# Optimization experiments

Measured on AMD Instinct MI355X. Metric: run time of the kernel, lower is better.

## Reference

```python
import jax, jax.numpy as jnp
import numpy as np

NUM_HEADS = 32
HEAD_DIM = 128
NUM_KV_HEADS = 8
Q_LEN = 1024
MAX_SEQ = 4096
CACHE_BATCH = 4
SEQ_POS = 1024
BATCH_POS = 1


def setup_inputs() -> dict:
    key = jax.random.key(0)
    ks = jax.random.split(key, 6)
    query_state = jax.random.normal(ks[0], (1, NUM_HEADS, Q_LEN, HEAD_DIM), jnp.float32)
    key_state = jax.random.normal(ks[1], (1, NUM_KV_HEADS, Q_LEN, HEAD_DIM), jnp.float32)
    value_state = jax.random.normal(ks[2], (1, NUM_KV_HEADS, Q_LEN, HEAD_DIM), jnp.float32)
    past_key_state = jax.random.normal(ks[3], (CACHE_BATCH, NUM_KV_HEADS, MAX_SEQ, HEAD_DIM), jnp.float32)
    past_value_state = jax.random.normal(ks[4], (CACHE_BATCH, NUM_KV_HEADS, MAX_SEQ, HEAD_DIM), jnp.float32)
    # Causal prefill mask: query token i (global pos SEQ_POS+i) may attend to cache pos m <= SEQ_POS+i
    i = jnp.arange(Q_LEN)[:, None] + SEQ_POS
    j = jnp.arange(MAX_SEQ)[None, :]
    attn_mask = (j <= i).astype(jnp.float32)[None, None]  # [1,1,Q_LEN,MAX_SEQ]
    scale = jnp.array([1.0 / np.sqrt(HEAD_DIM)], jnp.float32)
    return {
        "query_state": query_state,
        "key_state": key_state,
        "value_state": value_state,
        "attn_mask": attn_mask,
        "batch_position": BATCH_POS,
        "past_key_state": past_key_state,
        "past_value_state": past_value_state,
        "seq_position": SEQ_POS,
        "scale": scale,
    }


def reference(query_state, key_state, value_state, attn_mask, batch_position,
              past_key_state, past_value_state, seq_position, scale):
    g = NUM_HEADS // NUM_KV_HEADS
    q_len = query_state.shape[2]
    # --- cache update (prefill: insert new K/V at [batch_position, :, seq_position:seq_position+q_len]) ---
    k_cache = jax.lax.dynamic_update_slice(past_key_state, key_state, (batch_position, 0, seq_position, 0))
    v_cache = jax.lax.dynamic_update_slice(past_value_state, value_state, (batch_position, 0, seq_position, 0))
    # --- grouped-query attention over the updated cache row ---
    q = query_state.reshape(1, NUM_KV_HEADS, g, q_len, HEAD_DIM)
    k = jax.lax.dynamic_slice_in_dim(k_cache, batch_position, 1, axis=0)[0]  # [kvh, MAX_SEQ, hd]
    v = jax.lax.dynamic_slice_in_dim(v_cache, batch_position, 1, axis=0)[0]
    scores = jnp.einsum('bkgqd,kmd->bkgqm', q, k) * scale[0]  # [1,kvh,g,q,MAX_SEQ]
    neg = jnp.finfo(scores.dtype).min
    scores = jnp.where(attn_mask[:, :, None] > 0.5, scores, neg)
    probs = jax.nn.softmax(scores, axis=-1)
    out = jnp.einsum('bkgqm,kmd->bkgqd', probs, v)  # [1,kvh,g,q,hd]
    out = out.reshape(1, NUM_HEADS, q_len, HEAD_DIM)
    attn_output = out.transpose(0, 2, 1, 3).reshape(1, q_len, NUM_HEADS * HEAD_DIM)
    return attn_output, k_cache, v_cache
```

## Files before the change

kernel.cpp:

```cpp
#include <hip/hip_runtime.h>

#define NH 32
#define KVHN 8
#define HD 128
#define QL 1024
#define MS 4096
#define KVB 64

typedef __bf16 bf16x8 __attribute__((ext_vector_type(8)));
typedef __bf16 bf16x4 __attribute__((ext_vector_type(4)));
typedef float f32x4 __attribute__((ext_vector_type(4)));
typedef float f32x16 __attribute__((ext_vector_type(16)));


__device__ __forceinline__ void gload16(const void* g, void* l) {
    __builtin_amdgcn_global_load_lds(
        (const __attribute__((address_space(1))) unsigned int*)g,
        (__attribute__((address_space(3))) unsigned int*)l, 16, 0, 0);
}

__device__ __forceinline__ unsigned int pk2(float a, float b) {
    union { __bf16 h; unsigned short u; } x, y;
    x.h = (__bf16)a; y.h = (__bf16)b;
    return (unsigned int)x.u | ((unsigned int)y.u << 16);
}

__device__ __forceinline__ float exp2fast(float x) {
    return __builtin_amdgcn_exp2f(x);
}

__global__ __launch_bounds__(256) void pack_kernel(
    const float4* __restrict__ kn, const float4* __restrict__ vn,
    const float4* __restrict__ pk, const float4* __restrict__ pv,
    const int* __restrict__ bp_p, const int* __restrict__ sp_p,
    __bf16* __restrict__ kbf, __bf16* __restrict__ vt)
{
    __shared__ float vtile[8][132];
    int li = blockIdx.x * 256 + threadIdx.x;
    int bp = *bp_p, sp = *sp_p;
    int d4  = li & 31;
    int pos = (li >> 5) & 4095;
    int kvh = li >> 17;
    float4 kv4, vv4;
    if (pos >= sp && pos < sp + QL) {
        int ns = (kvh * QL + (pos - sp)) * 32 + d4;
        kv4 = kn[ns]; vv4 = vn[ns];
    } else {
        int gi = (bp << 20) + li;
        kv4 = pk[gi]; vv4 = pv[gi];
    }
    {
        bf16x4 o;
        o[0] = (__bf16)kv4.x; o[1] = (__bf16)kv4.y;
        o[2] = (__bf16)kv4.z; o[3] = (__bf16)kv4.w;
        int c16 = d4 >> 1, half = d4 & 1;
        *(bf16x4*)(kbf + ((size_t)kvh * MS + pos) * HD
                       + ((c16 ^ (pos & 7)) * 8 + half * 4)) = o;
        *(float4*)&vtile[threadIdx.x >> 5][d4 * 4] = vv4;
    }
    __syncthreads();
    if (threadIdx.x < 128) {
        int d  = threadIdx.x;
        int p0 = (blockIdx.x * 8) & 4095;
        int pt = p0 >> 6, chk = (p0 & 63) >> 3;
        bf16x8 o;
        #pragma unroll
        for (int j = 0; j < 8; ++j) o[j] = (__bf16)vtile[j][d];
        *(bf16x8*)(vt + (((size_t)kvh * 64 + pt) * HD + d) * 64
                      + ((chk ^ (d & 7)) * 8)) = o;
    }
}

__global__ __launch_bounds__(256, 2) void mega_kernel(
    const float* __restrict__ q,
    const int* __restrict__ bp_p, const int* __restrict__ sp_p,
    const float* __restrict__ scale_p,
    const __bf16* __restrict__ kbf, const __bf16* __restrict__ vt,
    const float4* __restrict__ knf, const float4* __restrict__ vnf,
    const float4* __restrict__ pkf, const float4* __restrict__ pvf,
    float4* __restrict__ okf, float4* __restrict__ ovf,
    float* __restrict__ out)
{
    __shared__ __align__(16) unsigned char smem[65536];

    const int bid = blockIdx.x;
    const int tid = threadIdx.x;
    const int sp  = *sp_p;
    const int bp  = *bp_p;

    if (bid >= 512) {
        int cslot = bid - 512;
        const float4* csrc_new  = (cslot < 256) ? knf : vnf;
        const float4* csrc_past = (cslot < 256) ? pkf : pvf;
        float4*       cdst      = (cslot < 256) ? okf : ovf;
        const int     cbase     = (cslot & 255) * 16384;
        for (int s = 0; s < 16; ++s) {
            float4 t[4];
            #pragma unroll
            for (int jj = 0; jj < 4; ++jj) {
                int idx = cbase + s * 1024 + jj * 256 + tid;
                int d4  = idx & 31;
                int pos = (idx >> 5) & 4095;
                int ck  = (idx >> 17) & 7;
                int b   = idx >> 20;
                t[jj] = (b == bp && pos >= sp && pos < sp + QL)
                    ? csrc_new[(ck * QL + (pos - sp)) * 32 + d4]
                    : csrc_past[idx];
            }
            #pragma unroll
            for (int jj = 0; jj < 4; ++jj)
                cdst[cbase + s * 1024 + jj * 256 + tid] = t[jj];
        }
        return;
    }

    const float scl = *scale_p * 1.44269504088896340736f;

    int kvh = bid & 7;
    int inner = (bid & 255) >> 3;
    int headLocal = inner & 3;
    int j = inner >> 2;
    int qtile = (bid < 256) ? j : 15 - j;
    int head = kvh * 4 + headLocal;

    const int q0     = qtile * 64;
    const int wave   = tid >> 6;
    const int qsub   = wave & 1;
    const int kvhalf = wave >> 1;
    const int lane   = tid & 63;
    const int hi     = lane >> 5;
    const int c31    = lane & 31;
    const int qb     = q0 + qsub * 32;
    const int myq    = qb + c31;

    const unsigned char* krow = (const unsigned char*)(kbf + (size_t)kvh * MS * HD);
    const unsigned char* vrow = (const unsigned char*)(vt + (size_t)kvh * 64 * HD * 64);

    bf16x8 qf[8];
    #pragma unroll
    for (int dc = 0; dc < 8; ++dc) {
        const float* src = q + ((size_t)(head * QL + qb + c31) * HD + dc * 16 + hi * 8);
        float4 f0 = *(const float4*)src;
        float4 f1 = *(const float4*)(src + 4);
        bf16x8 v;
        v[0]=(__bf16)(f0.x*scl); v[1]=(__bf16)(f0.y*scl);
        v[2]=(__bf16)(f0.z*scl); v[3]=(__bf16)(f0.w*scl);
        v[4]=(__bf16)(f1.x*scl); v[5]=(__bf16)(f1.y*scl);
        v[6]=(__bf16)(f1.z*scl); v[7]=(__bf16)(f1.w*scl);
        qf[dc] = v;
    }

    f32x16 acc[4];
    #pragma unroll
    for (int dsub = 0; dsub < 4; ++dsub)
        #pragma unroll
        for (int r = 0; r < 16; ++r) acc[dsub][r] = 0.f;
    float m_run = -1e30f, l_run = 0.f;

    const int n_super = (sp + q0 + 64) >> 6;

    auto stage = [&](int buf, int t) {
        const unsigned char* kt = krow + (size_t)t * 16384;
        const unsigned char* vtile = vrow + (size_t)t * 16384;
        unsigned char* kl = smem + buf * 32768;
        unsigned char* vl = kl + 16384;
        #pragma unroll
        for (int p = 0; p < 4; ++p) {
            int off = p * 4096 + tid * 16;
            gload16(kt + off, kl + off);
            gload16(vtile + off, vl + off);
        }
    };

    int cur = 0;
    stage(0, 0);
    __syncthreads();

    for (int it = 0; it < n_super; ++it) {
        const int n0 = it * KVB + kvhalf * 32;
        if (it + 1 < n_super) stage(cur ^ 1, it + 1);

        const unsigned char* Ksm = smem + cur * 32768;
        const unsigned char* Vsm = Ksm + 16384;

        f32x16 st0, st1;
        #pragma unroll
        for (int r = 0; r < 16; ++r) { st0[r] = 0.f; st1[r] = 0.f; }
        int kr = kvhalf * 32 + c31;
        __builtin_amdgcn_s_setprio(1);
        #pragma unroll
        for (int dc = 0; dc < 4; ++dc) {
            bf16x8 ka = *(const bf16x8*)(Ksm + kr * 256 + (((2 * dc + hi) ^ (kr & 7)) << 4));
            st0 = __builtin_amdgcn_mfma_f32_32x32x16_bf16(ka, qf[dc], st0, 0, 0, 0);
            bf16x8 kb = *(const bf16x8*)(Ksm + kr * 256 + (((2 * (dc + 4) + hi) ^ (kr & 7)) << 4));
            st1 = __builtin_amdgcn_mfma_f32_32x32x16_bf16(kb, qf[dc + 4], st1, 0, 0, 0);
        }
        __builtin_amdgcn_s_setprio(0);
        f32x16 st = st0 + st1;

        const bool need_mask = (n0 + 31) > (sp + qb);
        if (need_mask) {
            #pragma unroll
            for (int r = 0; r < 16; ++r) {
                int kvg = n0 + (r & 3) + 8 * (r >> 2) + 4 * hi;
                if (kvg > sp + myq) st[r] = -1e30f;
            }
        }
        float m01 = fmaxf(fmaxf(st[0], st[1]), fmaxf(st[2], st[3]));
        float m23 = fmaxf(fmaxf(st[4], st[5]), fmaxf(st[6], st[7]));
        float m45 = fmaxf(fmaxf(st[8], st[9]), fmaxf(st[10], st[11]));
        float m67 = fmaxf(fmaxf(st[12], st[13]), fmaxf(st[14], st[15]));
        float mx = fmaxf(fmaxf(m01, m23), fmaxf(m45, m67));
        mx = fmaxf(mx, __shfl_xor(mx, 32));

        if (!__all(mx <= m_run + 8.0f)) {
            float nm = fmaxf(m_run, mx);
            float corr = exp2fast(m_run - nm);
            m_run = nm;
            l_run *= corr;
            #pragma unroll
            for (int r = 0; r < 16; ++r) {
                int qsrc = (r & 3) + 8 * (r >> 2) + 4 * hi;
                float cq = __shfl(corr, qsrc);
                acc[0][r] *= cq; acc[1][r] *= cq; acc[2][r] *= cq; acc[3][r] *= cq;
            }
        }

        #pragma unroll
        for (int r = 0; r < 16; ++r) st[r] = exp2fast(st[r] - m_run);
        {
            float s0 = (st[0] + st[1]) + (st[2] + st[3]);
            float s1 = (st[4] + st[5]) + (st[6] + st[7]);
            float s2 = (st[8] + st[9]) + (st[10] + st[11]);
            float s3 = (st[12] + st[13]) + (st[14] + st[15]);
            l_run += (s0 + s1) + (s2 + s3);
        }

        unsigned int loW[4], hiW[4];
        #pragma unroll
        for (int qd = 0; qd < 2; ++qd) {
            int b = qd * 8;
            loW[qd*2+0] = pk2(st[b+0], st[b+1]);
            loW[qd*2+1] = pk2(st[b+2], st[b+3]);
            hiW[qd*2+0] = pk2(st[b+4], st[b+5]);
            hiW[qd*2+1] = pk2(st[b+6], st[b+7]);
        }
        bf16x8 pfrag[2];
        #pragma unroll
        for (int qd = 0; qd < 2; ++qd) {
            unsigned int a0 = loW[qd*2+0], b0 = hiW[qd*2+0];
            unsigned int a1 = loW[qd*2+1], b1 = hiW[qd*2+1];
            asm("v_permlane32_swap_b32 %0, %1" : "+v"(a0), "+v"(b0));
            asm("v_permlane32_swap_b32 %0, %1" : "+v"(a1), "+v"(b1));
            union { unsigned int u[4]; bf16x8 v; } fu;
            fu.u[0] = a0; fu.u[1] = a1; fu.u[2] = b0; fu.u[3] = b1;
            pfrag[qd] = fu.v;
        }

        __builtin_amdgcn_s_setprio(1);
        #pragma unroll
        for (int dsub = 0; dsub < 4; ++dsub) {
            int vr = dsub * 32 + c31;
            #pragma unroll
            for (int qd = 0; qd < 2; ++qd) {
                int ksg = kvhalf * 2 + qd;
                bf16x8 vf = *(const bf16x8*)(Vsm + vr * 128 + (((ksg * 2 + hi) ^ (vr & 7)) << 4));
                acc[dsub] = __builtin_amdgcn_mfma_f32_32x32x16_bf16(pfrag[qd], vf, acc[dsub], 0, 0, 0);
            }
        }
        __builtin_amdgcn_s_setprio(0);

        __syncthreads();
        cur ^= 1;
    }

    float l_full = l_run + __shfl_xor(l_run, 32);
    float* mlm = (float*)smem;
    float* mll = (float*)smem + 128;
    if (hi == 0) { mlm[wave * 32 + c31] = m_run; mll[wave * 32 + c31] = l_full; }
    __syncthreads();
    int pw = wave ^ 2;
    float m_o = mlm[pw * 32 + c31];
    float l_o = mll[pw * 32 + c31];
    float m_n = fmaxf(m_run, m_o);
    float sc   = exp2fast(m_run - m_n);
    float sc_o = exp2fast(m_o - m_n);
    float linv = 1.0f / (l_full * sc + l_o * sc_o);
    float* Oex = (float*)(smem + 1024) + (size_t)qsub * 32 * 128;
    if (kvhalf) {
        #pragma unroll
        for (int r = 0; r < 16; ++r) {
            int qsrc = (r & 3) + 8 * (r >> 2) + 4 * hi;
            float s = __shfl(sc, qsrc);
            #pragma unroll
            for (int dsub = 0; dsub < 4; ++dsub)
                Oex[qsrc * 128 + dsub * 32 + c31] = acc[dsub][r] * s;
        }
    }
    __syncthreads();
    if (!kvhalf) {
        #pragma unroll
        for (int r = 0; r < 16; ++r) {
            int qsrc = (r & 3) + 8 * (r >> 2) + 4 * hi;
            float s  = __shfl(sc, qsrc);
            float lq = __shfl(linv, qsrc);
            float* orow = out + (size_t)(qb + qsrc) * (NH * HD) + head * HD;
            #pragma unroll
            for (int dsub = 0; dsub < 4; ++dsub)
                orow[dsub * 32 + c31] =
                    (acc[dsub][r] * s + Oex[qsrc * 128 + dsub * 32 + c31]) * lq;
        }
    }
}

extern "C" void kernel_launch(void* const* d_in, const int* in_sizes, int n_in,
                              void* d_out, int out_size, void* d_ws, size_t ws_size,
                              hipStream_t stream)
{
    const float* q_st   = (const float*)d_in[0];
    const float* k_new  = (const float*)d_in[1];
    const float* v_new  = (const float*)d_in[2];
    const int*   bp_p   = (const int*)d_in[4];
    const float* past_k = (const float*)d_in[5];
    const float* past_v = (const float*)d_in[6];
    const int*   sp_p   = (const int*)d_in[7];
    const float* scl_p  = (const float*)d_in[8];

    float* out_attn = (float*)d_out;
    float* out_k    = out_attn + (size_t)QL * NH * HD;
    float* out_v    = out_k + (size_t)4 * KVHN * MS * HD;

    __bf16* kbf = (__bf16*)d_ws;
    __bf16* vtw = kbf + (size_t)KVHN * MS * HD;

    pack_kernel<<<4096, 256, 0, stream>>>(
        (const float4*)k_new, (const float4*)v_new,
        (const float4*)past_k, (const float4*)past_v,
        bp_p, sp_p, kbf, vtw);

    mega_kernel<<<1024, 256, 0, stream>>>(
        q_st, bp_p, sp_p, scl_p, kbf, vtw,
        (const float4*)k_new, (const float4*)v_new,
        (const float4*)past_k, (const float4*)past_v,
        (float4*)out_k, (float4*)out_v, out_attn);
}
```

Before: 105.6 us.

## Co-schedule cache copy waves inside attention blocks with nontemporal loads/stores

Replaces the separate 512 copy-only blocks with 512-thread blocks in which the upper 256 threads copy the KV cache slices while the lower 256 threads compute attention. The copy waves step through the attention loop's barriers so that copy traffic is spread over the attention mainloop, and they use nontemporal loads and stores to avoid polluting cache. The barrier counts have to match the attention path exactly, and the larger blocks change occupancy and register limits via launch_bounds(512,4).

```diff
diff --git a/kernel.cpp b/kernel.cpp
--- a/kernel.cpp
+++ b/kernel.cpp
@@ -11,6 +11,7 @@
 typedef __bf16 bf16x4 __attribute__((ext_vector_type(4)));
 typedef float f32x4 __attribute__((ext_vector_type(4)));
 typedef float f32x16 __attribute__((ext_vector_type(16)));
+typedef unsigned int u32x4 __attribute__((ext_vector_type(4)));
 
 
 __device__ __forceinline__ void gload16(const void* g, void* l) {
@@ -27,6 +28,13 @@
 
 __device__ __forceinline__ float exp2fast(float x) {
     return __builtin_amdgcn_exp2f(x);
+}
+
+__device__ __forceinline__ u32x4 nt_load(const u32x4* p) {
+    return __builtin_nontemporal_load(p);
+}
+__device__ __forceinline__ void nt_store(u32x4* p, u32x4 v) {
+    __builtin_nontemporal_store(v, p);
 }
 
 __global__ __launch_bounds__(256) void pack_kernel(
@@ -71,7 +79,7 @@
     }
 }
 
-__global__ __launch_bounds__(256, 2) void mega_kernel(
+__global__ __launch_bounds__(512, 4) void mega_kernel(
     const float* __restrict__ q,
     const int* __restrict__ bp_p, const int* __restrict__ sp_p,
     const float* __restrict__ scale_p,
@@ -88,42 +96,67 @@
     const int sp  = *sp_p;
     const int bp  = *bp_p;
 
-    if (bid >= 512) {
-        int cslot = bid - 512;
-        const float4* csrc_new  = (cslot < 256) ? knf : vnf;
-        const float4* csrc_past = (cslot < 256) ? pkf : pvf;
-        float4*       cdst      = (cslot < 256) ? okf : ovf;
-        const int     cbase     = (cslot & 255) * 16384;
-        for (int s = 0; s < 16; ++s) {
-            float4 t[4];
-            #pragma unroll
-            for (int jj = 0; jj < 4; ++jj) {
-                int idx = cbase + s * 1024 + jj * 256 + tid;
-                int d4  = idx & 31;
-                int pos = (idx >> 5) & 4095;
-                int ck  = (idx >> 17) & 7;
-                int b   = idx >> 20;
-                t[jj] = (b == bp && pos >= sp && pos < sp + QL)
-                    ? csrc_new[(ck * QL + (pos - sp)) * 32 + d4]
-                    : csrc_past[idx];
-            }
-            #pragma unroll
-            for (int jj = 0; jj < 4; ++jj)
-                cdst[cbase + s * 1024 + jj * 256 + tid] = t[jj];
-        }
-        return;
-    }
-
-    const float scl = *scale_p * 1.44269504088896340736f;
-
     int kvh = bid & 7;
     int inner = (bid & 255) >> 3;
     int headLocal = inner & 3;
     int j = inner >> 2;
     int qtile = (bid < 256) ? j : 15 - j;
     int head = kvh * 4 + headLocal;
-
-    const int q0     = qtile * 64;
+    const int q0 = qtile * 64;
+    const int n_super = (sp + q0 + 64) >> 6;
+
+    if (tid >= 256) {
+        const int ctid = tid - 256;
+        const u32x4* csrc_new  = (const u32x4*)((bid < 256) ? knf : vnf);
+        const u32x4* csrc_past = (const u32x4*)((bid < 256) ? pkf : pvf);
+        u32x4*       cdst      = (u32x4*)((bid < 256) ? okf : ovf);
+        const int    cbase     = (bid & 255) * 16384;
+
+        __syncthreads();
+        for (int it = 0; it < n_super; ++it) {
+            if (it < 16) {
+                u32x4 t[4];
+                #pragma unroll
+                for (int jj = 0; jj < 4; ++jj) {
+                    int idx = cbase + it * 1024 + jj * 256 + ctid;
+                    int d4  = idx & 31;
+                    int pos = (idx >> 5) & 4095;
+                    int ck  = (idx >> 17) & 7;
+                    int b   = idx >> 20;
+                    t[jj] = (b == bp && pos >= sp && pos < sp + QL)
+                        ? nt_load(&csrc_new[(ck * QL + (pos - sp)) * 32 + d4])
+                        : nt_load(&csrc_past[idx]);
+                }
+                #pragma unroll
+                for (int jj = 0; jj < 4; ++jj)
+                    nt_store(&cdst[cbase + it * 1024 + jj * 256 + ctid], t[jj]);
+            }
+            __syncthreads();
+        }
+        for (int s = n_super; s < 16; ++s) {
+            u32x4 t[4];
+            #pragma unroll
+            for (int jj = 0; jj < 4; ++jj) {
+                int idx = cbase + s * 1024 + jj * 256 + ctid;
+                int d4  = idx & 31;
+                int pos = (idx >> 5) & 4095;
+                int ck  = (idx >> 17) & 7;
+                int b   = idx >> 20;
+                t[jj] = (b == bp && pos >= sp && pos < sp + QL)
+                    ? nt_load(&csrc_new[(ck * QL + (pos - sp)) * 32 + d4])
+                    : nt_load(&csrc_past[idx]);
+            }
+            #pragma unroll
+            for (int jj = 0; jj < 4; ++jj)
+                nt_store(&cdst[cbase + s * 1024 + jj * 256 + ctid], t[jj]);
+        }
+        __syncthreads();
+        __syncthreads();
+        return;
+    }
+
+    const float scl = *scale_p * 1.44269504088896340736f;
+
     const int wave   = tid >> 6;
     const int qsub   = wave & 1;
     const int kvhalf = wave >> 1;
@@ -156,8 +189,6 @@
         #pragma unroll
         for (int r = 0; r < 16; ++r) acc[dsub][r] = 0.f;
     float m_run = -1e30f, l_run = 0.f;
-
-    const int n_super = (sp + q0 + 64) >> 6;
 
     auto stage = [&](int buf, int t) {
         const unsigned char* kt = krow + (size_t)t * 16384;
@@ -338,7 +369,7 @@
         (const float4*)past_k, (const float4*)past_v,
         bp_p, sp_p, kbf, vtw);
 
-    mega_kernel<<<1024, 256, 0, stream>>>(
+    mega_kernel<<<512, 512, 0, stream>>>(
         q_st, bp_p, sp_p, scl_p, kbf, vtw,
         (const float4*)k_new, (const float4*)v_new,
         (const float4*)past_k, (const float4*)past_v,
```

Result: slower. 165.4 us (+56.6%).

## Load V fragments directly from global, halve LDS, interleave copy blocks

Applied to the files above, without the earlier changes.

V tiles are no longer staged through LDS. Each wave reads its V MFMA fragments straight from global memory into registers at the start of every iteration, and only K keeps the LDS double buffer. Shared memory drops to 32 KB, which may let more blocks fit per CU. The cache-copy blocks are now interleaved with the attention blocks in the grid and use nontemporal loads and stores. The partial-output exchange between waves is stored as bf16, which cuts LDS space but lowers the precision of that half of the accumulator.

```diff
diff --git a/kernel.cpp b/kernel.cpp
--- a/kernel.cpp
+++ b/kernel.cpp
@@ -11,6 +11,7 @@
 typedef __bf16 bf16x4 __attribute__((ext_vector_type(4)));
 typedef float f32x4 __attribute__((ext_vector_type(4)));
 typedef float f32x16 __attribute__((ext_vector_type(16)));
+typedef unsigned int u32x4 __attribute__((ext_vector_type(4)));
 
 
 __device__ __forceinline__ void gload16(const void* g, void* l) {
@@ -27,6 +28,13 @@
 
 __device__ __forceinline__ float exp2fast(float x) {
     return __builtin_amdgcn_exp2f(x);
+}
+
+__device__ __forceinline__ u32x4 nt_load(const u32x4* p) {
+    return __builtin_nontemporal_load(p);
+}
+__device__ __forceinline__ void nt_store(u32x4* p, u32x4 v) {
+    __builtin_nontemporal_store(v, p);
 }
 
 __global__ __launch_bounds__(256) void pack_kernel(
@@ -81,21 +89,21 @@
     float4* __restrict__ okf, float4* __restrict__ ovf,
     float* __restrict__ out)
 {
-    __shared__ __align__(16) unsigned char smem[65536];
+    __shared__ __align__(16) unsigned char smem[32768];
 
     const int bid = blockIdx.x;
     const int tid = threadIdx.x;
     const int sp  = *sp_p;
     const int bp  = *bp_p;
 
-    if (bid >= 512) {
-        int cslot = bid - 512;
-        const float4* csrc_new  = (cslot < 256) ? knf : vnf;
-        const float4* csrc_past = (cslot < 256) ? pkf : pvf;
-        float4*       cdst      = (cslot < 256) ? okf : ovf;
-        const int     cbase     = (cslot & 255) * 16384;
+    if ((bid >> 8) & 1) {
+        int cslot = (bid < 512) ? (bid - 256) : (bid - 768) + 256;
+        const u32x4* csrc_new  = (const u32x4*)((cslot < 256) ? knf : vnf);
+        const u32x4* csrc_past = (const u32x4*)((cslot < 256) ? pkf : pvf);
+        u32x4*       cdst      = (u32x4*)((cslot < 256) ? okf : ovf);
+        const int    cbase     = (cslot & 255) * 16384;
         for (int s = 0; s < 16; ++s) {
-            float4 t[4];
+            u32x4 t[4];
             #pragma unroll
             for (int jj = 0; jj < 4; ++jj) {
                 int idx = cbase + s * 1024 + jj * 256 + tid;
@@ -104,23 +112,24 @@
                 int ck  = (idx >> 17) & 7;
                 int b   = idx >> 20;
                 t[jj] = (b == bp && pos >= sp && pos < sp + QL)
-                    ? csrc_new[(ck * QL + (pos - sp)) * 32 + d4]
-                    : csrc_past[idx];
+                    ? nt_load(&csrc_new[(ck * QL + (pos - sp)) * 32 + d4])
+                    : nt_load(&csrc_past[idx]);
             }
             #pragma unroll
             for (int jj = 0; jj < 4; ++jj)
-                cdst[cbase + s * 1024 + jj * 256 + tid] = t[jj];
+                nt_store(&cdst[cbase + s * 1024 + jj * 256 + tid], t[jj]);
         }
         return;
     }
 
+    const int attnIdx = (bid < 256) ? bid : bid - 256;
     const float scl = *scale_p * 1.44269504088896340736f;
 
-    int kvh = bid & 7;
-    int inner = (bid & 255) >> 3;
+    int kvh = attnIdx & 7;
+    int inner = (attnIdx & 255) >> 3;
     int headLocal = inner & 3;
     int j = inner >> 2;
-    int qtile = (bid < 256) ? j : 15 - j;
+    int qtile = (attnIdx < 256) ? j : 15 - j;
     int head = kvh * 4 + headLocal;
 
     const int q0     = qtile * 64;
@@ -159,29 +168,41 @@
 
     const int n_super = (sp + q0 + 64) >> 6;
 
-    auto stage = [&](int buf, int t) {
+    auto stageK = [&](int buf, int t) {
         const unsigned char* kt = krow + (size_t)t * 16384;
-        const unsigned char* vtile = vrow + (size_t)t * 16384;
-        unsigned char* kl = smem + buf * 32768;
-        unsigned char* vl = kl + 16384;
+        unsigned char* kl = smem + buf * 16384;
         #pragma unroll
         for (int p = 0; p < 4; ++p) {
             int off = p * 4096 + tid * 16;
             gload16(kt + off, kl + off);
-            gload16(vtile + off, vl + off);
         }
     };
 
     int cur = 0;
-    stage(0, 0);
+    stageK(0, 0);
     __syncthreads();
 
     for (int it = 0; it < n_super; ++it) {
         const int n0 = it * KVB + kvhalf * 32;
-        if (it + 1 < n_super) stage(cur ^ 1, it + 1);
-
-        const unsigned char* Ksm = smem + cur * 32768;
-        const unsigned char* Vsm = Ksm + 16384;
+
+        u32x4 vraw[4][2];
+        {
+            const unsigned char* vtb = vrow + (size_t)it * 16384;
+            #pragma unroll
+            for (int dsub = 0; dsub < 4; ++dsub) {
+                #pragma unroll
+                for (int qd = 0; qd < 2; ++qd) {
+                    int vr = dsub * 32 + c31;
+                    int ksg = kvhalf * 2 + qd;
+                    vraw[dsub][qd] = *(const u32x4*)(vtb + vr * 128
+                        + (((ksg * 2 + hi) ^ (vr & 7)) << 4));
+                }
+            }
+        }
+        __builtin_amdgcn_sched_barrier(0);
+        if (it + 1 < n_super) stageK(cur ^ 1, it + 1);
+
+        const unsigned char* Ksm = smem + cur * 16384;
 
         f32x16 st0, st1;
         #pragma unroll
@@ -260,12 +281,11 @@
         __builtin_amdgcn_s_setprio(1);
         #pragma unroll
         for (int dsub = 0; dsub < 4; ++dsub) {
-            int vr = dsub * 32 + c31;
             #pragma unroll
             for (int qd = 0; qd < 2; ++qd) {
-                int ksg = kvhalf * 2 + qd;
-                bf16x8 vf = *(const bf16x8*)(Vsm + vr * 128 + (((ksg * 2 + hi) ^ (vr & 7)) << 4));
-                acc[dsub] = __builtin_amdgcn_mfma_f32_32x32x16_bf16(pfrag[qd], vf, acc[dsub], 0, 0, 0);
+                union { u32x4 u; bf16x8 v; } cvt;
+                cvt.u = vraw[dsub][qd];
+                acc[dsub] = __builtin_amdgcn_mfma_f32_32x32x16_bf16(pfrag[qd], cvt.v, acc[dsub], 0, 0, 0);
             }
         }
         __builtin_amdgcn_s_setprio(0);
@@ -286,7 +306,7 @@
     float sc   = exp2fast(m_run - m_n);
     float sc_o = exp2fast(m_o - m_n);
     float linv = 1.0f / (l_full * sc + l_o * sc_o);
-    float* Oex = (float*)(smem + 1024) + (size_t)qsub * 32 * 128;
+    __bf16* Oex = (__bf16*)(smem + 1024) + (size_t)qsub * 32 * 128;
     if (kvhalf) {
         #pragma unroll
         for (int r = 0; r < 16; ++r) {
@@ -294,7 +314,7 @@
             float s = __shfl(sc, qsrc);
             #pragma unroll
             for (int dsub = 0; dsub < 4; ++dsub)
-                Oex[qsrc * 128 + dsub * 32 + c31] = acc[dsub][r] * s;
+                Oex[qsrc * 128 + dsub * 32 + c31] = (__bf16)(acc[dsub][r] * s);
         }
     }
     __syncthreads();
@@ -308,7 +328,7 @@
             #pragma unroll
             for (int dsub = 0; dsub < 4; ++dsub)
                 orow[dsub * 32 + c31] =
-                    (acc[dsub][r] * s + Oex[qsrc * 128 + dsub * 32 + c31]) * lq;
+                    (acc[dsub][r] * s + (float)Oex[qsrc * 128 + dsub * 32 + c31]) * lq;
         }
     }
 }
```

After: 103.4 us (median of 3 runs). 1.02x faster.
